# Optimization experiments

Hardware: AMD Instinct MI355X
Metric: run time of the kernel (lower is better)

The kernel has to match this reference:

```python
import jax, jax.numpy as jnp
import numpy as np

NC = 80            # number of classes (COCO)
NM = 32            # mask coefficients (YOLOv5-seg)
D = 4 + 1 + NC + NM
N_ANCHORS = 100800  # 1280x1280 input, strides 8/16/32, 3 anchors
CONF_THRES = 0.25
IOU_THRES = 0.45
MAX_DET = 300
TOPK = 4096        # fixed pre-NMS candidate budget (jit-compatible stand-in for boolean filter)


def setup_inputs() -> dict:
    key = jax.random.key(0)
    x = jax.random.uniform(key, (1, N_ANCHORS, D), dtype=jnp.float32)
    return {"x": x}


def _pairwise_iou(boxes):
    # boxes: [K, 4] in (y1, x1, y2, x2)
    y1, x1, y2, x2 = boxes[:, 0], boxes[:, 1], boxes[:, 2], boxes[:, 3]
    area = (y2 - y1) * (x2 - x1)
    iy1 = jnp.maximum(y1[:, None], y1[None, :])
    ix1 = jnp.maximum(x1[:, None], x1[None, :])
    iy2 = jnp.minimum(y2[:, None], y2[None, :])
    ix2 = jnp.minimum(x2[:, None], x2[None, :])
    inter = jnp.clip(iy2 - iy1, 0.0) * jnp.clip(ix2 - ix1, 0.0)
    union = area[:, None] + area[None, :] - inter
    return inter / jnp.maximum(union, 1e-9)


def reference(x):
    p = x[0]                                   # [N, D] (loop returns after first image)
    obj = p[:, 4]
    valid = obj > CONF_THRES                   # candidates = obj score > conf_thres
    cls_scores = p[:, 5:5 + NC] * obj[:, None] # scores = cls * obj
    scores = jnp.max(cls_scores, axis=1)
    classes = jnp.argmax(cls_scores, axis=1).astype(x.dtype)
    # xywh (center) -> yxyx
    xc, yc, w, h = p[:, 0], p[:, 1], p[:, 2], p[:, 3]
    yxyx = jnp.stack([yc - h * 0.5, xc - w * 0.5, yc + h * 0.5, xc + w * 0.5], axis=1)
    masks = p[:, 5 + NC:]                      # [N, NM]
    # replace torch's boolean-filter gather with fixed-size top-K over masked scores
    scores_m = jnp.where(valid, scores, -1.0)
    top_s, top_i = jax.lax.top_k(scores_m, TOPK)   # sorted desc, as torchvision nms requires
    b = yxyx[top_i]                            # [K, 4]
    keep0 = top_s > -0.5                       # only real candidates
    iou = _pairwise_iou(b)                     # [K, K]
    j_idx = jnp.arange(TOPK)

    def body(i, keep):
        sup = keep[i] & (iou[i] > IOU_THRES) & (j_idx > i)
        return keep & ~sup

    keep = jax.lax.fori_loop(0, TOPK, body, keep0)
    # pad/select top MAX_DET surviving detections (score -1.0 marks padding)
    sel_s = jnp.where(keep, top_s, -1.0)
    out_s, out_i = jax.lax.top_k(sel_s, MAX_DET)
    gi = top_i[out_i]
    return (yxyx[gi][None], classes[gi][None], out_s[None], masks[gi][None])
```

## Files before the change

### kernel.cpp

```cpp
#include <hip/hip_runtime.h>


constexpr int    N_ANCH = 100800;
constexpr int    DIMV   = 117;
constexpr int    NCLS   = 80;
constexpr int    TOPKN  = 4096;
constexpr int    MAXDET = 300;
constexpr int    KCAP   = 12288;
constexpr int    NBUCK  = 16384;
constexpr int    NSLICE = 32;

constexpr size_t WS_HIST   = 0;
constexpr size_t WS_SCORES = WS_HIST   + 65536ull * 4;
constexpr size_t WS_CLS    = WS_SCORES + 100800ull * 4;
constexpr size_t WS_SEL    = WS_CLS    + 100800ull * 4;
constexpr size_t WS_KEYS   = WS_SEL    + 256;
constexpr size_t WS_RANK   = WS_KEYS   + (size_t)KCAP * 8;
constexpr size_t WS_SIDX   = WS_RANK   + (size_t)KCAP * 4;
constexpr size_t WS_SSC    = WS_SIDX   + 4096ull * 4;
constexpr size_t WS_BOXES  = WS_SSC    + 4096ull * 4;
constexpr size_t WS_MASK   = WS_BOXES  + 4096ull * 16;
constexpr size_t WS_OUTI   = WS_MASK   + 4096ull * 64 * 8;
constexpr size_t WS_OUTS   = WS_OUTI   + 1200;

__global__ void zero_kernel(unsigned* __restrict__ slices, int* __restrict__ sel,
                            int* __restrict__ rank) {
    int i = blockIdx.x * blockDim.x + threadIdx.x;
    if (i < NSLICE * NBUCK) slices[i] = 0u;
    if (i < KCAP)           rank[i]  = 0;
    if (i < 64)             sel[i]   = 0;
}

constexpr int SROWS = 64;
__global__ void score_kernel(const float* __restrict__ x, float* __restrict__ scores,
                             int* __restrict__ cls, unsigned* __restrict__ slices) {
    __shared__ float sx[SROWS * DIMV];
    int block0 = blockIdx.x * SROWS;
    const float4* src = (const float4*)(x + (size_t)block0 * DIMV);
    float4* dst = (float4*)sx;
    constexpr int NV4 = SROWS * DIMV / 4;
    for (int i = threadIdx.x; i < NV4; i += 128) dst[i] = src[i];
    __syncthreads();
    int row  = threadIdx.x >> 1;
    int half = threadIdx.x & 1;
    const float* rp = sx + row * DIMV;
    float obj = rp[4];
    const float* cp = rp + 5 + half * 40;
    float best = -1.0f;
    int   bc   = half * 40;
#pragma unroll 8
    for (int c = 0; c < 40; ++c) {
        float s = __fmul_rn(cp[c], obj);
        if (s > best) { best = s; bc = half * 40 + c; }
    }
    float so = __shfl_xor(best, 1);
    int   co = __shfl_xor(bc, 1);
    if (half == 0) {
        if (so > best) { best = so; bc = co; }
        int a = block0 + row;
        bool valid = obj > 0.25f;
        scores[a] = valid ? best : -1.0f;
        cls[a]    = bc;
        if (valid) {
            unsigned b = __float_as_uint(best) >> 16;
            atomicAdd(&slices[(blockIdx.x & (NSLICE - 1)) * NBUCK + b], 1u);
        }
    }
}

__global__ void reduce_hist_kernel(const unsigned* __restrict__ slices,
                                   unsigned* __restrict__ hist) {
    int b = blockIdx.x * 256 + threadIdx.x;
    unsigned s = 0;
#pragma unroll
    for (int k = 0; k < NSLICE; ++k) s += slices[k * NBUCK + b];
    hist[b] = s;
}

__global__ void select_kernel(const unsigned* __restrict__ hist, int* sel) {
    __shared__ unsigned sv[1024];
    int t = threadIdx.x;
    int base = NBUCK - 16 * (t + 1);
    const uint4* hp = (const uint4*)(hist + base);
    unsigned own = 0;
#pragma unroll
    for (int k = 0; k < 4; ++k) {
        uint4 v = hp[k];
        own += v.x + v.y + v.z + v.w;
    }
    sv[t] = own;
    __syncthreads();
    for (int off = 1; off < 1024; off <<= 1) {
        unsigned v = (t >= off) ? sv[t - off] : 0u;
        __syncthreads();
        sv[t] += v;
        __syncthreads();
    }
    unsigned incl = sv[t];
    unsigned before = incl - own;
    if (before < (unsigned)TOPKN && incl >= (unsigned)TOPKN) {
        unsigned running = before;
        for (int k = 15; k >= 0; --k) {
            unsigned h = hist[base + k];
            running += h;
            if (running >= (unsigned)TOPKN) {
                sel[0] = base + k;
                sel[1] = (int)(running - h);
                break;
            }
        }
    }
}

__global__ void compact_kernel(const float* __restrict__ scores, int* sel,
                               unsigned long long* __restrict__ keys) {
    int a = blockIdx.x * blockDim.x + threadIdx.x;
    if (a >= N_ANCH) return;
    float s = scores[a];
    if (s < 0.0f) return;
    unsigned bits = __float_as_uint(s);
    if ((int)(bits >> 16) < sel[0]) return;
    int pos = atomicAdd(&sel[2], 1);
    if (pos < KCAP) keys[pos] = ((unsigned long long)bits << 32) | (unsigned)(~a);
}

constexpr int NCOLP = 4;
__global__ void rank_kernel(const unsigned long long* __restrict__ keys,
                            const int* __restrict__ sel, int* __restrict__ rank) {
    __shared__ unsigned long long tile[2048];
    int n = sel[2]; if (n > KCAP) n = KCAP;
    int i = blockIdx.x * 256 + threadIdx.x;
    unsigned long long myKey = (i < n) ? keys[i] : 0ull;
    int cnt = 0;
    for (int t0 = blockIdx.y * 2048; t0 < n; t0 += 2048 * NCOLP) {
        int m = n - t0; if (m > 2048) m = 2048;
        for (int j = threadIdx.x; j < m; j += 256) tile[j] = keys[t0 + j];
        __syncthreads();
        int j = 0;
        for (; j + 3 < m; j += 4) {
            cnt += (tile[j]     > myKey);
            cnt += (tile[j + 1] > myKey);
            cnt += (tile[j + 2] > myKey);
            cnt += (tile[j + 3] > myKey);
        }
        for (; j < m; ++j) cnt += (tile[j] > myKey);
        __syncthreads();
    }
    if (i < n && cnt < TOPKN) atomicAdd(&rank[i], cnt);
}

__global__ void scatter_kernel(const float* __restrict__ x,
                               const unsigned long long* __restrict__ keys,
                               const int* __restrict__ sel, const int* __restrict__ rank,
                               int* __restrict__ sidx, float* __restrict__ sscore,
                               float* __restrict__ boxes) {
    int n = sel[2]; if (n > KCAP) n = KCAP;
    int i = blockIdx.x * 256 + threadIdx.x;
    if (i >= n) return;
    int r = rank[i];
    if (r >= TOPKN) return;
    unsigned long long k = keys[i];
    int a = (int)(~(unsigned)(k & 0xFFFFFFFFull));
    sidx[r]   = a;
    sscore[r] = __uint_as_float((unsigned)(k >> 32));
    const float* p = x + (size_t)a * DIMV;
    float xc = p[0], yc = p[1], w = p[2], h = p[3];
    float hw = __fmul_rn(w, 0.5f);
    float hh = __fmul_rn(h, 0.5f);
    boxes[r * 4 + 0] = __fsub_rn(yc, hh);
    boxes[r * 4 + 1] = __fsub_rn(xc, hw);
    boxes[r * 4 + 2] = __fadd_rn(yc, hh);
    boxes[r * 4 + 3] = __fadd_rn(xc, hw);
}

__global__ void iou_mask_kernel(const float* __restrict__ boxes,
                                unsigned long long* __restrict__ mask) {
    int colT = blockIdx.x, rowT = blockIdx.y;
    int t = threadIdx.x;
    int r = rowT * 64 + t;
    if (colT < rowT) {
        mask[(size_t)r * 64 + colT] = 0ull;
        return;
    }
    __shared__ float cb[64][5];
    int cj = colT * 64 + t;
    {
        float y1 = boxes[cj * 4 + 0], x1 = boxes[cj * 4 + 1];
        float y2 = boxes[cj * 4 + 2], x2 = boxes[cj * 4 + 3];
        cb[t][0] = y1; cb[t][1] = x1; cb[t][2] = y2; cb[t][3] = x2;
        cb[t][4] = __fmul_rn(__fsub_rn(y2, y1), __fsub_rn(x2, x1));
    }
    __syncthreads();
    float ry1 = boxes[r * 4 + 0], rx1 = boxes[r * 4 + 1];
    float ry2 = boxes[r * 4 + 2], rx2 = boxes[r * 4 + 3];
    float rarea = __fmul_rn(__fsub_rn(ry2, ry1), __fsub_rn(rx2, rx1));
    unsigned long long bitsw = 0ull;
#pragma unroll 8
    for (int j = 0; j < 64; ++j) {
        float iy1 = fmaxf(ry1, cb[j][0]);
        float ix1 = fmaxf(rx1, cb[j][1]);
        float iy2 = fminf(ry2, cb[j][2]);
        float ix2 = fminf(rx2, cb[j][3]);
        float ih = fmaxf(__fsub_rn(iy2, iy1), 0.0f);
        float iw = fmaxf(__fsub_rn(ix2, ix1), 0.0f);
        float inter = __fmul_rn(ih, iw);
        float uni = __fsub_rn(__fadd_rn(rarea, cb[j][4]), inter);
        float iou = __fdiv_rn(inter, fmaxf(uni, 1e-9f));
        if (iou > 0.45f && (colT * 64 + j) > r) bitsw |= (1ull << j);
    }
    mask[(size_t)r * 64 + colT] = bitsw;
}

__global__ void __launch_bounds__(64, 1)
nms_scan_kernel(const unsigned long long* __restrict__ mask,
                const float* __restrict__ sscore,
                int* __restrict__ outIdx, float* __restrict__ outScore) {
    constexpr int BATCH = 64;
    int lane = threadIdx.x;
    unsigned long long remv = 0ull;
    __shared__ int list[BATCH];
    __shared__ int keepArr[MAXDET];
    __shared__ unsigned long long remvFinal[64];
    int count = 0;
    int pos = 0;
    while (count < MAXDET && pos < TOPKN) {
        unsigned long long avail = ~remv;
        int w0 = pos >> 6;
        if (lane < w0) avail = 0ull;
        else if (lane == w0) avail &= (~0ull) << (pos & 63);
        int cnt = __popcll(avail);
        int pre = cnt;
        for (int off = 1; off < 64; off <<= 1) {
            int v = __shfl_up(pre, off);
            if (lane >= off) pre += v;
        }
        int total = __shfl(pre, 63);
        pre -= cnt;
        unsigned long long a = avail;
        int slot = pre;
        while (a && slot < BATCH) {
            int b = (int)__builtin_ctzll(a);
            a &= a - 1;
            list[slot] = (lane << 6) + b;
            slot++;
        }
        __syncthreads();
        int nb = (total < BATCH) ? total : BATCH;
        if (nb == 0) break;
        int rows[BATCH];
        unsigned long long m[BATCH];
#pragma unroll
        for (int k = 0; k < BATCH; ++k) {
            if (k < nb) rows[k] = list[k];
        }
#pragma unroll
        for (int k = 0; k < BATCH; ++k) {
            if (k < nb) m[k] = mask[(size_t)rows[k] * 64 + lane];
        }
        int lastRow = list[0];
#pragma unroll
        for (int k = 0; k < BATCH; ++k) {
            if (k < nb && count < MAXDET) {
                int r = rows[k];
                lastRow = r;
                unsigned long long bal = __ballot(((remv >> (r & 63)) & 1ull) != 0);
                if (!((bal >> (r >> 6)) & 1ull)) {
                    if (lane == 0) keepArr[count] = r;
                    count++;
                    remv |= m[k];
                }
            }
        }
        pos = lastRow + 1;
        __syncthreads();
    }
    remvFinal[lane] = remv;
    __syncthreads();
    int K = count;
    for (int k = lane; k < K; k += 64) {
        int s = keepArr[k];
        outIdx[k] = s;
        outScore[k] = sscore[s];
    }
    if (K < MAXDET && lane == 0) {
        int filled = K;
        for (int w = 0; w < 64 && filled < MAXDET; ++w) {
            unsigned long long word = remvFinal[w];
            while (word && filled < MAXDET) {
                int b = (int)__builtin_ctzll(word);
                word &= word - 1;
                outIdx[filled] = (w << 6) + b;
                outScore[filled] = -1.0f;
                filled++;
            }
        }
    }
}

__global__ void write_out_kernel(const float* __restrict__ x, const int* __restrict__ sidx,
                                 const int* __restrict__ cls, const float* __restrict__ boxes,
                                 const int* __restrict__ outIdx, const float* __restrict__ outScore,
                                 float* __restrict__ out) {
    int o = blockIdx.x;
    int t = threadIdx.x;
    int s = outIdx[o];
    int a = sidx[s];
    if (t < 32) {
        out[1800 + o * 32 + t] = x[(size_t)a * DIMV + 85 + t];
    } else if (t < 36) {
        out[o * 4 + (t - 32)] = boxes[s * 4 + (t - 32)];
    } else if (t == 36) {
        out[1200 + o] = (float)cls[a];
    } else if (t == 37) {
        out[1500 + o] = outScore[o];
    }
}

extern "C" void kernel_launch(void* const* d_in, const int* in_sizes, int n_in,
                              void* d_out, int out_size, void* d_ws, size_t ws_size,
                              hipStream_t stream) {
    const float* x = (const float*)d_in[0];
    char* ws = (char*)d_ws;
    unsigned*            hist   = (unsigned*)(ws + WS_HIST);
    float*               scores = (float*)(ws + WS_SCORES);
    int*                 cls    = (int*)(ws + WS_CLS);
    int*                 sel    = (int*)(ws + WS_SEL);
    unsigned long long*  keys   = (unsigned long long*)(ws + WS_KEYS);
    int*                 rank   = (int*)(ws + WS_RANK);
    int*                 sidx   = (int*)(ws + WS_SIDX);
    float*               sscore = (float*)(ws + WS_SSC);
    float*               boxes  = (float*)(ws + WS_BOXES);
    unsigned long long*  mask   = (unsigned long long*)(ws + WS_MASK);
    unsigned*            slices = (unsigned*)(ws + WS_MASK);
    int*                 outIdx = (int*)(ws + WS_OUTI);
    float*               outSc  = (float*)(ws + WS_OUTS);

    zero_kernel<<<(NSLICE * NBUCK + 255) / 256, 256, 0, stream>>>(slices, sel, rank);
    score_kernel<<<N_ANCH / SROWS, 128, 0, stream>>>(x, scores, cls, slices);
    reduce_hist_kernel<<<NBUCK / 256, 256, 0, stream>>>(slices, hist);
    select_kernel<<<1, 1024, 0, stream>>>(hist, sel);
    compact_kernel<<<(N_ANCH + 255) / 256, 256, 0, stream>>>(scores, sel, keys);
    dim3 rg(KCAP / 256, NCOLP);
    rank_kernel<<<rg, 256, 0, stream>>>(keys, sel, rank);
    scatter_kernel<<<KCAP / 256, 256, 0, stream>>>(x, keys, sel, rank, sidx, sscore, boxes);
    dim3 mg(64, 64);
    iou_mask_kernel<<<mg, 64, 0, stream>>>(boxes, mask);
    nms_scan_kernel<<<1, 64, 0, stream>>>(mask, sscore, outIdx, outSc);
    write_out_kernel<<<MAXDET, 64, 0, stream>>>(x, sidx, cls, boxes, outIdx, outSc, (float*)d_out);
}
```

Before: 232.1 us.

## Double-buffer NMS mask row blocks into LDS with async global_load_lds

Replaces the compacted candidate gather in the serial NMS scan with block-wise streaming. Each 64-row chunk of the suppression bitmask is prefetched into LDS through `global_load_lds`, double-buffered so the next chunk loads while the current one is scanned. Rows are read from LDS in groups of 8, which cuts dependent global-load latency on the single-wave critical path. In exchange it loads whole blocks including suppressed rows, uses 64KB of LDS, and relies on `__syncthreads` to cover completion of the async LDS loads.

```diff
diff --git a/kernel.cpp b/kernel.cpp
--- a/kernel.cpp
+++ b/kernel.cpp
@@ -1,5 +1,8 @@
 #include <hip/hip_runtime.h>
 
+
+#define AS1 __attribute__((address_space(1)))
+#define AS3 __attribute__((address_space(3)))
 
 constexpr int    N_ANCH = 100800;
 constexpr int    DIMV   = 117;
@@ -215,65 +218,61 @@
 nms_scan_kernel(const unsigned long long* __restrict__ mask,
                 const float* __restrict__ sscore,
                 int* __restrict__ outIdx, float* __restrict__ outScore) {
-    constexpr int BATCH = 64;
     int lane = threadIdx.x;
     unsigned long long remv = 0ull;
-    __shared__ int list[BATCH];
+    __shared__ __align__(16) unsigned long long tile[2 * 4096];
     __shared__ int keepArr[MAXDET];
     __shared__ unsigned long long remvFinal[64];
     int count = 0;
-    int pos = 0;
-    while (count < MAXDET && pos < TOPKN) {
-        unsigned long long avail = ~remv;
-        int w0 = pos >> 6;
-        if (lane < w0) avail = 0ull;
-        else if (lane == w0) avail &= (~0ull) << (pos & 63);
-        int cnt = __popcll(avail);
-        int pre = cnt;
-        for (int off = 1; off < 64; off <<= 1) {
-            int v = __shfl_up(pre, off);
-            if (lane >= off) pre += v;
-        }
-        int total = __shfl(pre, 63);
-        pre -= cnt;
-        unsigned long long a = avail;
-        int slot = pre;
-        while (a && slot < BATCH) {
-            int b = (int)__builtin_ctzll(a);
-            a &= a - 1;
-            list[slot] = (lane << 6) + b;
-            slot++;
-        }
-        __syncthreads();
-        int nb = (total < BATCH) ? total : BATCH;
-        if (nb == 0) break;
-        int rows[BATCH];
-        unsigned long long m[BATCH];
-#pragma unroll
-        for (int k = 0; k < BATCH; ++k) {
-            if (k < nb) rows[k] = list[k];
-        }
-#pragma unroll
-        for (int k = 0; k < BATCH; ++k) {
-            if (k < nb) m[k] = mask[(size_t)rows[k] * 64 + lane];
-        }
-        int lastRow = list[0];
-#pragma unroll
-        for (int k = 0; k < BATCH; ++k) {
-            if (k < nb && count < MAXDET) {
-                int r = rows[k];
-                lastRow = r;
-                unsigned long long bal = __ballot(((remv >> (r & 63)) & 1ull) != 0);
-                if (!((bal >> (r >> 6)) & 1ull)) {
-                    if (lane == 0) keepArr[count] = r;
-                    count++;
-                    remv |= m[k];
+
+    auto issueBatch = [&](int w, int buf) {
+        const char* gbase = (const char*)mask + (size_t)w * 32768 + (size_t)lane * 16;
+        char* lbase = (char*)tile + (size_t)buf * 32768;
+#pragma unroll
+        for (int i = 0; i < 32; ++i) {
+            __builtin_amdgcn_global_load_lds(
+                (AS1 const unsigned*)(gbase + (size_t)i * 1024),
+                (AS3 unsigned*)(lbase + (size_t)i * 1024), 16, 0, 0);
+        }
+    };
+
+    issueBatch(0, 0);
+    for (int w = 0; w < 64 && count < MAXDET; ++w) {
+        if (w + 1 < 64) issueBatch(w + 1, (w + 1) & 1);
+        unsigned long long cand = __shfl(~remv, w);
+        if (!cand) continue;
+        __syncthreads();
+        const unsigned long long* trow = tile + (size_t)(w & 1) * 4096;
+        while (cand && count < MAXDET) {
+            int bs[8];
+            unsigned long long c2 = cand;
+            int g = 0;
+#pragma unroll
+            for (int t = 0; t < 8; ++t) {
+                bs[t] = c2 ? (int)__builtin_ctzll(c2) : 0;
+                if (c2) { c2 &= c2 - 1; g = t + 1; }
+            }
+            unsigned long long mvs[8];
+#pragma unroll
+            for (int t = 0; t < 8; ++t) {
+                mvs[t] = trow[(size_t)bs[t] * 64 + lane];
+            }
+#pragma unroll
+            for (int t = 0; t < 8; ++t) {
+                if (t < g && count < MAXDET) {
+                    int b = bs[t];
+                    unsigned long long bal = __ballot(((remv >> b) & 1ull) != 0);
+                    if (!((bal >> w) & 1ull)) {
+                        if (lane == 0) keepArr[count] = (w << 6) + b;
+                        count++;
+                        remv |= mvs[t];
+                    }
                 }
             }
-        }
-        pos = lastRow + 1;
-        __syncthreads();
-    }
+            cand = c2;
+        }
+    }
+    __syncthreads();
     remvFinal[lane] = remv;
     __syncthreads();
     int K = count;
```

New measurement: 218.1 us. 1.06x faster.
